# Performance work log

Hardware: AMD Instinct MI355X
Metric: run time of the kernel (lower is better)

The kernel has to match this reference:

```python
import jax, jax.numpy as jnp
import numpy as np

INNER_DIM = 256
DT_SIZE = 64
STATE_DIM = 256  # must equal INNER_DIM for the original split() to be valid
BATCH, SEQ_LEN = 2, 512


def setup_inputs() -> dict:
    key = jax.random.key(0)
    k_x, k_win, k_wdt, k_bdt = jax.random.split(key, 4)
    x = jax.random.normal(k_x, (BATCH, SEQ_LEN, INNER_DIM), dtype=jnp.float32)
    # nn.Linear(inner_dim, dt_size + 2*state_dim, bias=False); stored as [in, out] for x @ W
    W_in = jax.random.normal(k_win, (INNER_DIM, DT_SIZE + 2 * STATE_DIM), dtype=jnp.float32) / np.sqrt(INNER_DIM)
    # nn.Linear(dt_size, inner_dim) with bias
    W_dt = jax.random.normal(k_wdt, (DT_SIZE, INNER_DIM), dtype=jnp.float32) / np.sqrt(DT_SIZE)
    b_dt = jax.random.normal(k_bdt, (INNER_DIM,), dtype=jnp.float32) * 0.01
    # alpha_log = log(repeat(arange(1, N+1), 'n -> d n'))
    alpha_log = jnp.log(jnp.broadcast_to(
        jnp.arange(1, STATE_DIM + 1, dtype=jnp.float32), (INNER_DIM, STATE_DIM)))
    delta = jnp.ones((INNER_DIM,), dtype=jnp.float32)
    return {"input_tensor": x, "W_in": W_in, "W_dt": W_dt, "b_dt": b_dt,
            "alpha_log": alpha_log, "delta": delta}


def reference(input_tensor, W_in, W_dt, b_dt, alpha_log, delta):
    x = input_tensor
    alpha = -jnp.exp(alpha_log)  # [D, N]
    proj = x @ W_in  # [B, L, DT + 2D]
    dt_raw, beta, gamma = jnp.split(proj, [DT_SIZE, DT_SIZE + INNER_DIM], axis=-1)
    dt = jax.nn.softplus(dt_raw @ W_dt + b_dt)  # [B, L, D]
    # dt_a = exp(dt[...,None] * alpha) : [B, L, D, N]
    dt_a = jnp.exp(jnp.einsum('bld,dn->bldn', dt, alpha))
    # dt_b_i = dt * x outer beta : [B, L, D, N]
    dt_b_i = jnp.einsum('bld,bln->bldn', dt * x, beta)

    def step(state, inputs):
        a_t, b_t, g_t = inputs  # [B,D,N], [B,D,N], [B,N]
        state = a_t * state + b_t
        y_t = jnp.einsum('bdn,bn->bd', state, g_t)
        return state, y_t

    s0 = jnp.zeros((x.shape[0], INNER_DIM, STATE_DIM), dtype=x.dtype)
    _, ys = jax.lax.scan(step, s0, (jnp.moveaxis(dt_a, 1, 0),
                                    jnp.moveaxis(dt_b_i, 1, 0),
                                    jnp.moveaxis(gamma, 1, 0)))
    ys = jnp.moveaxis(ys, 0, 1)  # [B, L, D]
    return ys + x * delta
```

## Files before the change

kernel.cpp:

```cpp
#include <hip/hip_runtime.h>
#include <math.h>

#define DIM   256
#define NST   256
#define LSEQ  512
#define BAT   2
#define DTSZ  64
#define PCOLS 576
#define NROWS 1024

constexpr float LOG2E = 1.4426950408889634f;

__device__ __forceinline__ float fexp2(float v) {
#if __has_builtin(__builtin_amdgcn_exp2f)
    return __builtin_amdgcn_exp2f(v);
#else
    return exp2f(v);
#endif
}

__device__ __forceinline__ float softplusf(float v) {
    return (v > 20.f) ? v : log1pf(__expf(v));
}

__device__ __forceinline__ void barrier_lds_only() {
    __builtin_amdgcn_s_waitcnt(0xC07F);
    __builtin_amdgcn_s_barrier();
}

__device__ __forceinline__ unsigned pack_bg(float be, float ga) {
    unsigned ub = __float_as_uint(be);
    unsigned ug = __float_as_uint(ga);
    ub = (ub + 0x7fffu + ((ub >> 16) & 1u)) >> 16;
    ug = (ug + 0x7fffu + ((ug >> 16) & 1u)) & 0xffff0000u;
    return ub | ug;
}

__global__ __launch_bounds__(256) void proj_kernel(
    const float* __restrict__ x, const float* __restrict__ W_in,
    const float* __restrict__ W_dt, const float* __restrict__ b_dt,
    unsigned* __restrict__ betgam,
    float* __restrict__ dtp, float* __restrict__ dtxp)
{
    __shared__ float xs[2][DIM];
    __shared__ float draw[2][DTSZ];
    const int j = threadIdx.x;
    const int row0 = blockIdx.x * 2;

    #pragma unroll
    for (int r = 0; r < 2; ++r) xs[r][j] = x[(row0 + r) * DIM + j];
    __syncthreads();

    float acc0[2] = {0.f, 0.f}, acc1[2] = {0.f, 0.f}, acc2[2] = {0.f, 0.f};
    const bool has2 = (j < 64);

    for (int kk = 0; kk < DIM; kk += 16) {
        float w0[16], w1[16], w2[16];
        #pragma unroll
        for (int u = 0; u < 16; ++u) {
            const int k = kk + u;
            w0[u] = W_in[k * PCOLS + j];
            w1[u] = W_in[k * PCOLS + 256 + j];
            w2[u] = has2 ? W_in[k * PCOLS + 512 + j] : 0.f;
        }
        #pragma unroll
        for (int r = 0; r < 2; ++r) {
            #pragma unroll
            for (int q = 0; q < 4; ++q) {
                float4 xv = *(const float4*)&xs[r][kk + q * 4];
                const float xa[4] = {xv.x, xv.y, xv.z, xv.w};
                #pragma unroll
                for (int u = 0; u < 4; ++u) {
                    const int uu = q * 4 + u;
                    acc0[r] = fmaf(xa[u], w0[uu], acc0[r]);
                    acc1[r] = fmaf(xa[u], w1[uu], acc1[r]);
                    acc2[r] = fmaf(xa[u], w2[uu], acc2[r]);
                }
            }
        }
    }

    #pragma unroll
    for (int r = 0; r < 2; ++r) {
        const int row = row0 + r;
        if (has2) {
            draw[r][j] = acc0[r];
            betgam[row * NST + 192 + j] = pack_bg(acc1[r], acc2[r]);
        } else {
            betgam[row * NST + (j - 64)] = pack_bg(acc0[r], acc1[r]);
        }
    }
    __syncthreads();

    float bd = b_dt[j];
    float accd[2] = {bd, bd};
    #pragma unroll 16
    for (int k = 0; k < DTSZ; ++k) {
        float w = W_dt[k * DIM + j];
        #pragma unroll
        for (int r = 0; r < 2; ++r) accd[r] = fmaf(draw[r][k], w, accd[r]);
    }
    #pragma unroll
    for (int r = 0; r < 2; ++r) {
        const int row = row0 + r;
        float sp = softplusf(accd[r]);
        dtp[row * DIM + j]  = sp;
        dtxp[row * DIM + j] = sp * xs[r][j];
    }
}

__global__ __launch_bounds__(256) void scan1p(
    const float* __restrict__ x,
    const float* __restrict__ alpha_log,
    const float* __restrict__ delta,
    const unsigned* __restrict__ betgam,
    const float* __restrict__ dtp,
    const float* __restrict__ dtxp,
    float* __restrict__ out)
{
    __shared__ float part[32][NST];
    __shared__ float dts[LSEQ], dxs[LSEQ];
    const int n = threadIdx.x;
    const int xcd  = blockIdx.x & 7;
    const int slot = blockIdx.x >> 3;
    const int b = xcd >> 2;
    const int d = slot * 4 + (xcd & 3);
    const int rb = b * LSEQ;

    #pragma unroll
    for (int it = 0; it < 2; ++it) {
        const int l = n + it * 256;
        dts[l] = dtp [(rb + l) * DIM + d];
        dxs[l] = dtxp[(rb + l) * DIM + d];
    }
    const float aln = -__expf(alpha_log[d * NST + n]) * LOG2E;
    const float dv  = delta[d];
    __syncthreads();

    float s = 0.f;
    unsigned bg[4][8];
    #pragma unroll
    for (int pw = 0; pw < 3; ++pw) {
        #pragma unroll
        for (int t = 0; t < 8; ++t)
            bg[pw][t] = betgam[(rb + pw * 8 + t) * NST + n];
    }

    #pragma unroll 4
    for (int w = 0; w < 64; ++w) {
        const int cur = w & 3;
        const int pf  = (w + 3) & 3;
        if (w + 3 < 64) {
            #pragma unroll
            for (int t = 0; t < 8; ++t)
                bg[pf][t] = betgam[(rb + (w + 3) * 8 + t) * NST + n];
        }
        float4 dta = *(const float4*)&dts[w * 8];
        float4 dtb = *(const float4*)&dts[w * 8 + 4];
        float4 dxa = *(const float4*)&dxs[w * 8];
        float4 dxb = *(const float4*)&dxs[w * 8 + 4];
        const float dtw[8] = {dta.x, dta.y, dta.z, dta.w, dtb.x, dtb.y, dtb.z, dtb.w};
        const float dxw[8] = {dxa.x, dxa.y, dxa.z, dxa.w, dxb.x, dxb.y, dxb.z, dxb.w};

        const int prow = (w & 3) * 8;
        #pragma unroll
        for (int t = 0; t < 8; ++t) {
            const unsigned u = bg[cur][t];
            const float be = __uint_as_float(u << 16);
            const float ga = __uint_as_float(u & 0xffff0000u);
            float a = fexp2(dtw[t] * aln);
            s = fmaf(a, s, dxw[t] * be);
            part[prow + t][n] = s * ga;
        }

        if ((w & 3) == 3) {
            barrier_lds_only();
            const int trow = n >> 3, seg = n & 7;
            float sum = 0.f;
            #pragma unroll
            for (int k = 0; k < 32; ++k)
                sum += part[trow][seg * 32 + ((k + n) & 31)];
            sum += __shfl_xor(sum, 1);
            sum += __shfl_xor(sum, 2);
            sum += __shfl_xor(sum, 4);
            if (seg == 0) {
                const int r = rb + (w >> 2) * 32 + trow;
                const int oidx = r * DIM + d;
                out[oidx] = sum + x[oidx] * dv;
            }
            barrier_lds_only();
        }
    }
}

extern "C" void kernel_launch(void* const* d_in, const int* in_sizes, int n_in,
                              void* d_out, int out_size, void* d_ws, size_t ws_size,
                              hipStream_t stream) {
    const float* x         = (const float*)d_in[0];
    const float* W_in      = (const float*)d_in[1];
    const float* W_dt      = (const float*)d_in[2];
    const float* b_dt      = (const float*)d_in[3];
    const float* alpha_log = (const float*)d_in[4];
    const float* delta     = (const float*)d_in[5];
    float* out = (float*)d_out;

    unsigned* betgam = (unsigned*)d_ws;
    float* dtp  = (float*)(betgam + NROWS * NST);
    float* dtxp = dtp + NROWS * DIM;

    proj_kernel<<<NROWS / 2, 256, 0, stream>>>(x, W_in, W_dt, b_dt, betgam, dtp, dtxp);
    scan1p<<<BAT * DIM, 256, 0, stream>>>(x, alpha_log, delta, betgam, dtp, dtxp, out);
}
```

Before: 119.3 us.

## Warp-specialize scan kernel with double-buffered LDS reduction by consumer waves

The scan kernel now launches 512 threads. The first 256 threads run the sequential state recurrence and write partial products into one of two LDS buffers. The other 256 threads reduce the previous buffer over the state dimension and write the output, so the reduction overlaps the next chunk of the recurrence instead of stalling it. The x column is also preloaded into LDS. The cost is doubled LDS for the partial buffer and larger blocks, which may reduce occupancy.

```diff
diff --git a/kernel.cpp b/kernel.cpp
--- a/kernel.cpp
+++ b/kernel.cpp
@@ -109,7 +109,7 @@
     }
 }
 
-__global__ __launch_bounds__(256) void scan1p(
+__global__ __launch_bounds__(512, 4) void scan1p(
     const float* __restrict__ x,
     const float* __restrict__ alpha_log,
     const float* __restrict__ delta,
@@ -118,75 +118,85 @@
     const float* __restrict__ dtxp,
     float* __restrict__ out)
 {
-    __shared__ float part[32][NST];
-    __shared__ float dts[LSEQ], dxs[LSEQ];
-    const int n = threadIdx.x;
+    __shared__ float part[2][32][NST];
+    __shared__ float dts[LSEQ], dxs[LSEQ], xcol[LSEQ];
+    const int tid = threadIdx.x;
     const int xcd  = blockIdx.x & 7;
     const int slot = blockIdx.x >> 3;
     const int b = xcd >> 2;
     const int d = slot * 4 + (xcd & 3);
     const int rb = b * LSEQ;
 
-    #pragma unroll
-    for (int it = 0; it < 2; ++it) {
-        const int l = n + it * 256;
-        dts[l] = dtp [(rb + l) * DIM + d];
-        dxs[l] = dtxp[(rb + l) * DIM + d];
-    }
-    const float aln = -__expf(alpha_log[d * NST + n]) * LOG2E;
-    const float dv  = delta[d];
+    dts[tid]  = dtp [(rb + tid) * DIM + d];
+    dxs[tid]  = dtxp[(rb + tid) * DIM + d];
+    xcol[tid] = x   [(rb + tid) * DIM + d];
+    const float dv = delta[d];
     __syncthreads();
 
-    float s = 0.f;
-    unsigned bg[4][8];
-    #pragma unroll
-    for (int pw = 0; pw < 3; ++pw) {
-        #pragma unroll
-        for (int t = 0; t < 8; ++t)
-            bg[pw][t] = betgam[(rb + pw * 8 + t) * NST + n];
-    }
-
-    #pragma unroll 4
-    for (int w = 0; w < 64; ++w) {
-        const int cur = w & 3;
-        const int pf  = (w + 3) & 3;
-        if (w + 3 < 64) {
+    if (tid < 256) {
+        const int n = tid;
+        const float aln = -__expf(alpha_log[d * NST + n]) * LOG2E;
+        float s = 0.f;
+        unsigned bg[4][8];
+        #pragma unroll
+        for (int pw = 0; pw < 3; ++pw) {
             #pragma unroll
             for (int t = 0; t < 8; ++t)
-                bg[pf][t] = betgam[(rb + (w + 3) * 8 + t) * NST + n];
-        }
-        float4 dta = *(const float4*)&dts[w * 8];
-        float4 dtb = *(const float4*)&dts[w * 8 + 4];
-        float4 dxa = *(const float4*)&dxs[w * 8];
-        float4 dxb = *(const float4*)&dxs[w * 8 + 4];
-        const float dtw[8] = {dta.x, dta.y, dta.z, dta.w, dtb.x, dtb.y, dtb.z, dtb.w};
-        const float dxw[8] = {dxa.x, dxa.y, dxa.z, dxa.w, dxb.x, dxb.y, dxb.z, dxb.w};
-
-        const int prow = (w & 3) * 8;
-        #pragma unroll
-        for (int t = 0; t < 8; ++t) {
-            const unsigned u = bg[cur][t];
-            const float be = __uint_as_float(u << 16);
-            const float ga = __uint_as_float(u & 0xffff0000u);
-            float a = fexp2(dtw[t] * aln);
-            s = fmaf(a, s, dxw[t] * be);
-            part[prow + t][n] = s * ga;
-        }
-
-        if ((w & 3) == 3) {
+                bg[pw][t] = betgam[(rb + pw * 8 + t) * NST + n];
+        }
+
+        for (int k = 0; k <= 16; ++k) {
+            if (k < 16) {
+                const int buf = k & 1;
+                #pragma unroll
+                for (int wi = 0; wi < 4; ++wi) {
+                    const int w = k * 4 + wi;
+                    const int cur = w & 3;
+                    const int pf  = (w + 3) & 3;
+                    if (w + 3 < 64) {
+                        #pragma unroll
+                        for (int t = 0; t < 8; ++t)
+                            bg[pf][t] = betgam[(rb + (w + 3) * 8 + t) * NST + n];
+                    }
+                    float4 dta = *(const float4*)&dts[w * 8];
+                    float4 dtb = *(const float4*)&dts[w * 8 + 4];
+                    float4 dxa = *(const float4*)&dxs[w * 8];
+                    float4 dxb = *(const float4*)&dxs[w * 8 + 4];
+                    const float dtw[8] = {dta.x, dta.y, dta.z, dta.w,
+                                          dtb.x, dtb.y, dtb.z, dtb.w};
+                    const float dxw[8] = {dxa.x, dxa.y, dxa.z, dxa.w,
+                                          dxb.x, dxb.y, dxb.z, dxb.w};
+                    #pragma unroll
+                    for (int t = 0; t < 8; ++t) {
+                        const unsigned u = bg[cur][t];
+                        const float be = __uint_as_float(u << 16);
+                        const float ga = __uint_as_float(u & 0xffff0000u);
+                        float a = fexp2(dtw[t] * aln);
+                        s = fmaf(a, s, dxw[t] * be);
+                        part[buf][wi * 8 + t][n] = s * ga;
+                    }
+                }
+            }
             barrier_lds_only();
-            const int trow = n >> 3, seg = n & 7;
-            float sum = 0.f;
-            #pragma unroll
-            for (int k = 0; k < 32; ++k)
-                sum += part[trow][seg * 32 + ((k + n) & 31)];
-            sum += __shfl_xor(sum, 1);
-            sum += __shfl_xor(sum, 2);
-            sum += __shfl_xor(sum, 4);
-            if (seg == 0) {
-                const int r = rb + (w >> 2) * 32 + trow;
-                const int oidx = r * DIM + d;
-                out[oidx] = sum + x[oidx] * dv;
+        }
+    } else {
+        const int ct = tid - 256;
+        const int trow = ct >> 3;
+        const int seg  = ct & 7;
+        for (int k = 0; k <= 16; ++k) {
+            if (k >= 1) {
+                const int buf = (k - 1) & 1;
+                float sum = 0.f;
+                #pragma unroll
+                for (int kk = 0; kk < 32; ++kk)
+                    sum += part[buf][trow][seg * 32 + ((kk + ct) & 31)];
+                sum += __shfl_xor(sum, 1);
+                sum += __shfl_xor(sum, 2);
+                sum += __shfl_xor(sum, 4);
+                if (seg == 0) {
+                    const int l = (k - 1) * 32 + trow;
+                    out[(rb + l) * DIM + d] = sum + xcol[l] * dv;
+                }
             }
             barrier_lds_only();
         }
@@ -209,5 +219,5 @@
     float* dtxp = dtp + NROWS * DIM;
 
     proj_kernel<<<NROWS / 2, 256, 0, stream>>>(x, W_in, W_dt, b_dt, betgam, dtp, dtxp);
-    scan1p<<<BAT * DIM, 256, 0, stream>>>(x, alpha_log, delta, betgam, dtp, dtxp, out);
-}
+    scan1p<<<BAT * DIM, 512, 0, stream>>>(x, alpha_log, delta, betgam, dtp, dtxp, out);
+}
```

Result: no change. 119.2 us (-0.0%).

## Transpose dt buffers, pack partial outputs as bf16 pairs, stage x column in LDS

Applied to the files above, without the earlier changes.

The projection kernel now writes dt and dt*x transposed (column-major per channel), so the scan kernel reads them directly from global memory as uniform contiguous loads instead of first staging them in LDS with strided gathers. The per-step partial products are truncated to bf16 and packed two per word, which halves the LDS traffic and the footprint of the reduction buffer, and the reduction is reorganised to produce two outputs per group. The x column is preloaded into LDS for the residual term, and launch bounds request 2 blocks per CU. The cost is lower precision in the output sums from bf16 truncation, plus uncoalesced transposed stores in the projection kernel.

```diff
diff --git a/kernel.cpp b/kernel.cpp
--- a/kernel.cpp
+++ b/kernel.cpp
@@ -36,11 +36,20 @@
     return ub | ug;
 }
 
+__device__ __forceinline__ unsigned pack_trunc2(float a, float b) {
+#if __has_builtin(__builtin_amdgcn_perm)
+    return __builtin_amdgcn_perm(__float_as_uint(b), __float_as_uint(a), 0x07060302u);
+#else
+    return (__float_as_uint(a) >> 16) | (__float_as_uint(b) & 0xffff0000u);
+#endif
+}
+
 __global__ __launch_bounds__(256) void proj_kernel(
     const float* __restrict__ x, const float* __restrict__ W_in,
     const float* __restrict__ W_dt, const float* __restrict__ b_dt,
     unsigned* __restrict__ betgam,
-    float* __restrict__ dtp, float* __restrict__ dtxp)
+    float* __restrict__ dtT,
+    float* __restrict__ dtxT)
 {
     __shared__ float xs[2][DIM];
     __shared__ float draw[2][DTSZ];
@@ -104,22 +113,22 @@
     for (int r = 0; r < 2; ++r) {
         const int row = row0 + r;
         float sp = softplusf(accd[r]);
-        dtp[row * DIM + j]  = sp;
-        dtxp[row * DIM + j] = sp * xs[r][j];
-    }
-}
-
-__global__ __launch_bounds__(256) void scan1p(
+        dtT [j * NROWS + row] = sp;
+        dtxT[j * NROWS + row] = sp * xs[r][j];
+    }
+}
+
+__global__ __launch_bounds__(256, 2) void scan1p(
     const float* __restrict__ x,
     const float* __restrict__ alpha_log,
     const float* __restrict__ delta,
     const unsigned* __restrict__ betgam,
-    const float* __restrict__ dtp,
-    const float* __restrict__ dtxp,
+    const float* __restrict__ dtT,
+    const float* __restrict__ dtxT,
     float* __restrict__ out)
 {
-    __shared__ float part[32][NST];
-    __shared__ float dts[LSEQ], dxs[LSEQ];
+    __shared__ unsigned partp[16][NST];
+    __shared__ float xcol[LSEQ];
     const int n = threadIdx.x;
     const int xcd  = blockIdx.x & 7;
     const int slot = blockIdx.x >> 3;
@@ -130,11 +139,12 @@
     #pragma unroll
     for (int it = 0; it < 2; ++it) {
         const int l = n + it * 256;
-        dts[l] = dtp [(rb + l) * DIM + d];
-        dxs[l] = dtxp[(rb + l) * DIM + d];
+        xcol[l] = x[(rb + l) * DIM + d];
     }
     const float aln = -__expf(alpha_log[d * NST + n]) * LOG2E;
     const float dv  = delta[d];
+    const float* dtc = dtT  + (size_t)d * NROWS + rb;
+    const float* dxc = dtxT + (size_t)d * NROWS + rb;
     __syncthreads();
 
     float s = 0.f;
@@ -155,14 +165,14 @@
             for (int t = 0; t < 8; ++t)
                 bg[pf][t] = betgam[(rb + (w + 3) * 8 + t) * NST + n];
         }
-        float4 dta = *(const float4*)&dts[w * 8];
-        float4 dtb = *(const float4*)&dts[w * 8 + 4];
-        float4 dxa = *(const float4*)&dxs[w * 8];
-        float4 dxb = *(const float4*)&dxs[w * 8 + 4];
-        const float dtw[8] = {dta.x, dta.y, dta.z, dta.w, dtb.x, dtb.y, dtb.z, dtb.w};
-        const float dxw[8] = {dxa.x, dxa.y, dxa.z, dxa.w, dxb.x, dxb.y, dxb.z, dxb.w};
-
-        const int prow = (w & 3) * 8;
+        float dtw[8], dxw[8];
+        #pragma unroll
+        for (int t = 0; t < 8; ++t) {
+            dtw[t] = dtc[w * 8 + t];
+            dxw[t] = dxc[w * 8 + t];
+        }
+
+        float sy[8];
         #pragma unroll
         for (int t = 0; t < 8; ++t) {
             const unsigned u = bg[cur][t];
@@ -170,23 +180,32 @@
             const float ga = __uint_as_float(u & 0xffff0000u);
             float a = fexp2(dtw[t] * aln);
             s = fmaf(a, s, dxw[t] * be);
-            part[prow + t][n] = s * ga;
-        }
+            sy[t] = s * ga;
+        }
+        const int prow = (w & 3) * 4;
+        #pragma unroll
+        for (int t2 = 0; t2 < 4; ++t2)
+            partp[prow + t2][n] = pack_trunc2(sy[2 * t2], sy[2 * t2 + 1]);
 
         if ((w & 3) == 3) {
             barrier_lds_only();
-            const int trow = n >> 3, seg = n & 7;
-            float sum = 0.f;
+            const int pr  = n >> 4;
+            const int seg = n & 15;
+            float sum0 = 0.f, sum1 = 0.f;
             #pragma unroll
-            for (int k = 0; k < 32; ++k)
-                sum += part[trow][seg * 32 + ((k + n) & 31)];
-            sum += __shfl_xor(sum, 1);
-            sum += __shfl_xor(sum, 2);
-            sum += __shfl_xor(sum, 4);
+            for (int k = 0; k < 16; ++k) {
+                const unsigned u = partp[pr][seg * 16 + ((k + n) & 15)];
+                sum0 += __uint_as_float(u << 16);
+                sum1 += __uint_as_float(u & 0xffff0000u);
+            }
+            sum0 += __shfl_xor(sum0, 1);  sum1 += __shfl_xor(sum1, 1);
+            sum0 += __shfl_xor(sum0, 2);  sum1 += __shfl_xor(sum1, 2);
+            sum0 += __shfl_xor(sum0, 4);  sum1 += __shfl_xor(sum1, 4);
+            sum0 += __shfl_xor(sum0, 8);  sum1 += __shfl_xor(sum1, 8);
             if (seg == 0) {
-                const int r = rb + (w >> 2) * 32 + trow;
-                const int oidx = r * DIM + d;
-                out[oidx] = sum + x[oidx] * dv;
+                const int l0 = (w >> 2) * 32 + 2 * pr;
+                out[(rb + l0) * DIM + d]     = sum0 + xcol[l0] * dv;
+                out[(rb + l0 + 1) * DIM + d] = sum1 + xcol[l0 + 1] * dv;
             }
             barrier_lds_only();
         }
@@ -205,9 +224,9 @@
     float* out = (float*)d_out;
 
     unsigned* betgam = (unsigned*)d_ws;
-    float* dtp  = (float*)(betgam + NROWS * NST);
-    float* dtxp = dtp + NROWS * DIM;
-
-    proj_kernel<<<NROWS / 2, 256, 0, stream>>>(x, W_in, W_dt, b_dt, betgam, dtp, dtxp);
-    scan1p<<<BAT * DIM, 256, 0, stream>>>(x, alpha_log, delta, betgam, dtp, dtxp, out);
-}
+    float* dtT  = (float*)(betgam + NROWS * NST);
+    float* dtxT = dtT + NROWS * DIM;
+
+    proj_kernel<<<NROWS / 2, 256, 0, stream>>>(x, W_in, W_dt, b_dt, betgam, dtT, dtxT);
+    scan1p<<<BAT * DIM, 256, 0, stream>>>(x, alpha_log, delta, betgam, dtT, dtxT, out);
+}
```

New measurement: 126.4 us. 6.0% more time.
